# Kernel optimization log

Measured on AMD Instinct MI355X. Metric: run time of the kernel, lower is better.

Reference implementation:

```python
import jax, jax.numpy as jnp
import numpy as np

N = 50000      # nodes
E = 800000     # edges (before self-loops)
IN = 128
HID = 128
OUT = 64
L = 8          # num_layers
ALPHA = 0.1
THETA = 0.5
BN_EPS = 1e-5


def setup_inputs() -> dict:
    key = jax.random.key(0)
    ks = jax.random.split(key, 8)
    x = jax.random.normal(ks[0], (N, IN), dtype=jnp.float32)
    edge_index = jax.random.randint(ks[1], (2, E), 0, N, dtype=jnp.int32)
    # nn.Linear default init: U(-1/sqrt(fan_in), 1/sqrt(fan_in))
    s0 = 1.0 / np.sqrt(IN)
    lin0_w = jax.random.uniform(ks[2], (HID, IN), jnp.float32, -s0, s0)
    lin0_b = jax.random.uniform(ks[3], (HID,), jnp.float32, -s0, s0)
    s1 = 1.0 / np.sqrt(HID)
    lin1_w = jax.random.uniform(ks[4], (OUT, HID), jnp.float32, -s1, s1)
    lin1_b = jax.random.uniform(ks[5], (OUT,), jnp.float32, -s1, s1)
    # GCN2Conv weight1: glorot, shape [HID, HID], applied as h @ W
    g = np.sqrt(6.0 / (HID + HID))
    conv_w = jax.random.uniform(ks[6], (L, HID, HID), jnp.float32, -g, g)
    bn_gamma = jnp.ones((L, HID), jnp.float32)
    bn_beta = jnp.zeros((L, HID), jnp.float32)
    return {"x": x, "edge_index": edge_index, "lin0_w": lin0_w, "lin0_b": lin0_b,
            "lin1_w": lin1_w, "lin1_b": lin1_b, "conv_w": conv_w,
            "bn_gamma": bn_gamma, "bn_beta": bn_beta}


def _gcn_norm(edge_index):
    """PyG gcn_norm with add_self_loops=True, improved=False."""
    loops = jnp.arange(N, dtype=edge_index.dtype)
    src = jnp.concatenate([edge_index[0], loops])
    dst = jnp.concatenate([edge_index[1], loops])
    w = jnp.ones(src.shape[0], jnp.float32)
    deg = jax.ops.segment_sum(w, dst, num_segments=N)
    dinv = jnp.where(deg > 0, jax.lax.rsqrt(jnp.maximum(deg, 1e-12)), 0.0)
    norm = dinv[src] * w * dinv[dst]
    return src, dst, norm


def reference(x, edge_index, lin0_w, lin0_b, lin1_w, lin1_b, conv_w, bn_gamma, bn_beta):
    src, dst, norm = _gcn_norm(edge_index)
    # input projection (dropout is identity in eval/reference mode)
    h = jax.nn.relu(x @ lin0_w.T + lin0_b)
    h0 = h
    for i in range(L):
        # sparse adjacency propagation: out[dst] += norm * h[src]
        agg = jax.ops.segment_sum(norm[:, None] * h[src], dst, num_segments=N)
        # GCN2Conv with shared weights, normalize=False
        z = (1.0 - ALPHA) * agg + ALPHA * h0
        beta = float(np.log(THETA / (i + 1) + 1.0))
        z = (1.0 - beta) * z + beta * (z @ conv_w[i])
        # BatchNorm1d over nodes (batch statistics, biased variance)
        mean = z.mean(axis=0)
        var = z.var(axis=0)
        z = (z - mean) * jax.lax.rsqrt(var + BN_EPS) * bn_gamma[i] + bn_beta[i]
        h = jax.nn.relu(z)
    return h @ lin1_w.T + lin1_b
```

## Files before the change

kernel.cpp:

```cpp
#include <hip/hip_runtime.h>
#include <hip/hip_bf16.h>
#include <math.h>

#define N_NODES 50000
#define N_EDGES 800000
#define NLAYERS 8
#define ALPHA_C 0.1f
#define BN_EPS  1e-5f

typedef unsigned short u16;
typedef __attribute__((ext_vector_type(8))) short short8;
typedef __attribute__((ext_vector_type(4))) float f32x4;

static __device__ __forceinline__ u16 f2bf(float f) {
    unsigned u = __float_as_uint(f);
    unsigned r = (u + 0x7fffu + ((u >> 16) & 1u)) >> 16;
    return (u16)r;
}
static __device__ __forceinline__ float bf2f(u16 b) {
    return __uint_as_float((unsigned)b << 16);
}

__global__ __launch_bounds__(256) void k_init(int* cnt, int* fill, float* stats) {
    int i = blockIdx.x * 256 + threadIdx.x;
    if (i < N_NODES) { cnt[i] = 0; fill[i] = 0; }
    if (i < NLAYERS * 256) stats[i] = 0.0f;
}

__global__ __launch_bounds__(256) void k_count(const int* __restrict__ dst, int* cnt) {
    int e = blockIdx.x * 256 + threadIdx.x;
    if (e < N_EDGES) atomicAdd(&cnt[dst[e]], 1);
}

__global__ __launch_bounds__(256) void k_dinv(const int* __restrict__ cnt, float* __restrict__ dinv) {
    int i = blockIdx.x * 256 + threadIdx.x;
    if (i < N_NODES) dinv[i] = rsqrtf((float)(cnt[i] + 1));
}

__global__ __launch_bounds__(1024) void k_scan_local(const int* __restrict__ cnt,
                                                     int* __restrict__ rowptr, int* __restrict__ bsum) {
    __shared__ int tmp[1024];
    int t = threadIdx.x;
    int i = blockIdx.x * 1024 + t;
    int v = (i < N_NODES) ? cnt[i] : 0;
    tmp[t] = v;
    __syncthreads();
    for (int off = 1; off < 1024; off <<= 1) {
        int y = (t >= off) ? tmp[t - off] : 0;
        __syncthreads();
        tmp[t] += y;
        __syncthreads();
    }
    if (i < N_NODES) rowptr[i] = tmp[t] - v;
    if (t == 1023) bsum[blockIdx.x] = tmp[t];
}

__global__ void k_scan_top(int* bsum) {
    __shared__ int tmp[64];
    int t = threadIdx.x;
    int v = (t < 49) ? bsum[t] : 0;
    tmp[t] = v;
    __syncthreads();
    for (int off = 1; off < 64; off <<= 1) {
        int y = (t >= off) ? tmp[t - off] : 0;
        __syncthreads();
        tmp[t] += y;
        __syncthreads();
    }
    if (t < 49) bsum[t] = tmp[t] - v;
}

__global__ __launch_bounds__(256) void k_scan_add(int* __restrict__ rowptr, const int* __restrict__ bsum) {
    int i = blockIdx.x * 256 + threadIdx.x;
    if (i < N_NODES) rowptr[i] += bsum[i >> 10];
    if (i == 0) rowptr[N_NODES] = N_EDGES;
}

__global__ __launch_bounds__(256) void k_scatter(const int* __restrict__ src, const int* __restrict__ dst,
                                                 const int* __restrict__ rowptr, int* fill,
                                                 u16* __restrict__ ssrc) {
    int e = blockIdx.x * 256 + threadIdx.x;
    if (e < N_EDGES) {
        int d = dst[e];
        int pos = rowptr[d] + atomicAdd(&fill[d], 1);
        ssrc[pos] = (u16)src[e];
    }
}

__global__ __launch_bounds__(256) void k_convw(const float* __restrict__ conv_w,
                                               const float* __restrict__ lin0_w,
                                               const float* __restrict__ lin1_w,
                                               u16* __restrict__ wtb) {
    int t = blockIdx.x * 256 + threadIdx.x;
    if (t < 131072) {
        int j = (t >> 7) & 127, k = t & 127;
        int i = t >> 14;
        float v = conv_w[(i << 14) + (k << 7) + j];
        wtb[(t & ~127) | (k ^ ((j & 7) << 3))] = f2bf(v);
    } else if (t < 131072 + 16384) {
        int u = t - 131072;
        int j = u >> 7, k = u & 127;
        wtb[131072 + ((u & ~127) | (k ^ ((j & 7) << 3)))] = f2bf(lin0_w[u]);
    } else if (t < 131072 + 16384 + 8192) {
        int u = t - 147456;
        int j = u >> 7, k = u & 127;
        wtb[147456 + ((u & ~127) | (k ^ ((j & 7) << 3)))] = f2bf(lin1_w[u]);
    }
}

__global__ __launch_bounds__(256) void k_convx(const float* __restrict__ x, u16* __restrict__ xb) {
    size_t i = ((size_t)blockIdx.x * 256 + threadIdx.x) * 4;
    int row = (int)(i >> 7), j = (int)(i & 127);
    float4 v = *(const float4*)(x + i);
    uint2 o;
    o.x = (unsigned)f2bf(v.x) | ((unsigned)f2bf(v.y) << 16);
    o.y = (unsigned)f2bf(v.z) | ((unsigned)f2bf(v.w) << 16);
    *(uint2*)(xb + ((size_t)(j >> 4) * N_NODES + row) * 16 + (j & 15)) = o;
}

template<int NT, int MODE>
__global__ __launch_bounds__(256) void k_gemm_mfma(const u16* __restrict__ A,
                                                   const u16* __restrict__ Wg,
                                                   const float* __restrict__ bias,
                                                   float* __restrict__ Zf,
                                                   u16* __restrict__ h0b,
                                                   u16* __restrict__ hbp,
                                                   float* __restrict__ outF,
                                                   float* __restrict__ stats,
                                                   const float* __restrict__ dinv,
                                                   float beta_c, int M) {
    __shared__ u16 Ws[NT * 16 * 128];
    __shared__ float sstat[256];
    int tid = threadIdx.x;

    {
        const float4* srcv = (const float4*)Wg;
        float4* dstv = (float4*)Ws;
#pragma unroll
        for (int i = 0; i < NT; ++i) dstv[tid + i * 256] = srcv[tid + i * 256];
    }
    if (MODE == 1) sstat[tid] = 0.f;

    int wave = tid >> 6, lane = tid & 63;
    int r0 = blockIdx.x * 64 + wave * 16;
    int kg = lane >> 4;
    int cl = lane & 15;

    int arow = r0 + cl;
    int acl = arow < M ? arow : M - 1;
    short8 afrag[4];
#pragma unroll
    for (int kk = 0; kk < 4; ++kk) {
        int s = kk * 2 + (kg >> 1);
        afrag[kk] = *(const short8*)(A + ((size_t)s * N_NODES + acl) * 16 + (kg & 1) * 8);
    }

    __syncthreads();

    f32x4 acc[NT];
#pragma unroll
    for (int nt = 0; nt < NT; ++nt) {
        acc[nt] = (f32x4){0.f, 0.f, 0.f, 0.f};
        int j = nt * 16 + cl;
        const u16* wrow = Ws + j * 128;
        int sw = (j & 7) << 3;
#pragma unroll
        for (int kk = 0; kk < 4; ++kk) {
            short8 b = *(const short8*)(wrow + ((kk * 32 + kg * 8) ^ sw));
            acc[nt] = __builtin_amdgcn_mfma_f32_16x16x32_bf16(afrag[kk], b, acc[nt], 0, 0, 0);
        }
    }

    int rbase = r0 + kg * 4;
    float dvr[4];
    if (MODE != 1) {
#pragma unroll
        for (int reg = 0; reg < 4; ++reg) {
            int row = rbase + reg;
            dvr[reg] = (row < M) ? dinv[row] : 1.f;
        }
    }

#pragma unroll
    for (int nt = 0; nt < NT; ++nt) {
        int j = nt * 16 + cl;
        float s = 0.f, ss = 0.f;
#pragma unroll
        for (int reg = 0; reg < 4; ++reg) {
            int row = rbase + reg;
            if (row >= M) continue;
            float v = acc[nt][reg];
            size_t idx = ((size_t)nt * N_NODES + row) * 16 + cl;
            if (MODE == 0) {
                v = fmaxf(v + bias[j], 0.f);
                h0b[idx] = f2bf(v);
                hbp[idx] = f2bf(v * dvr[reg]);
            } else if (MODE == 1) {
                float zin = bf2f(A[idx]);
                v = (1.0f - beta_c) * zin + beta_c * v;
                Zf[idx] = v;
                s += v;
                ss = fmaf(v, v, ss);
            } else {
                outF[(size_t)row * (NT * 16) + j] = v / dvr[reg] + bias[j];
            }
        }
        if (MODE == 1) {
            s  += __shfl_xor(s, 16);  s  += __shfl_xor(s, 32);
            ss += __shfl_xor(ss, 16); ss += __shfl_xor(ss, 32);
            if (kg == 0) {
                atomicAdd(&sstat[j], s);
                atomicAdd(&sstat[128 + j], ss);
            }
        }
    }
    if (MODE == 1) {
        __syncthreads();
        atomicAdd(&stats[tid], sstat[tid]);
    }
}

__global__ __launch_bounds__(256) void k_aggregate(const u16* __restrict__ hbp, const u16* __restrict__ h0b,
                                                   const int* __restrict__ rowptr, const u16* __restrict__ ssrc,
                                                   const float* __restrict__ dinv,
                                                   u16* __restrict__ Zb) {
    int slice = blockIdx.x & 7;
    int wave = threadIdx.x >> 6, lane = threadIdx.x & 63;
    int rg = lane >> 3, lg = lane & 7;
    int v = (blockIdx.x >> 3) * 32 + wave * 8 + rg;
    if (v >= N_NODES) return;
    const u16* hs = hbp + (size_t)slice * (N_NODES * 16);
    int beg = rowptr[v], end = rowptr[v + 1];

    float ax, ay;
    {
        unsigned u = *(const unsigned*)(hs + (size_t)v * 16 + lg * 2);
        ax = __uint_as_float(u << 16);
        ay = __uint_as_float(u & 0xffff0000u);
    }
    int p = beg;
    for (; p + 4 <= end; p += 4) {
        int s0 = ssrc[p], s1 = ssrc[p + 1], s2 = ssrc[p + 2], s3 = ssrc[p + 3];
        unsigned u0 = *(const unsigned*)(hs + (size_t)s0 * 16 + lg * 2);
        unsigned u1 = *(const unsigned*)(hs + (size_t)s1 * 16 + lg * 2);
        unsigned u2 = *(const unsigned*)(hs + (size_t)s2 * 16 + lg * 2);
        unsigned u3 = *(const unsigned*)(hs + (size_t)s3 * 16 + lg * 2);
        ax += __uint_as_float(u0 << 16); ay += __uint_as_float(u0 & 0xffff0000u);
        ax += __uint_as_float(u1 << 16); ay += __uint_as_float(u1 & 0xffff0000u);
        ax += __uint_as_float(u2 << 16); ay += __uint_as_float(u2 & 0xffff0000u);
        ax += __uint_as_float(u3 << 16); ay += __uint_as_float(u3 & 0xffff0000u);
    }
    for (; p < end; ++p) {
        int s = ssrc[p];
        unsigned u = *(const unsigned*)(hs + (size_t)s * 16 + lg * 2);
        ax += __uint_as_float(u << 16); ay += __uint_as_float(u & 0xffff0000u);
    }

    float dv = dinv[v];
    unsigned uh = *(const unsigned*)(h0b + ((size_t)slice * N_NODES + v) * 16 + lg * 2);
    float zx = (1.0f - ALPHA_C) * dv * ax + ALPHA_C * __uint_as_float(uh << 16);
    float zy = (1.0f - ALPHA_C) * dv * ay + ALPHA_C * __uint_as_float(uh & 0xffff0000u);
    *(unsigned*)(Zb + ((size_t)slice * N_NODES + v) * 16 + lg * 2) =
        (unsigned)f2bf(zx) | ((unsigned)f2bf(zy) << 16);
}

__global__ __launch_bounds__(256) void k_bn_relu(const float* __restrict__ Zf, const float* __restrict__ stats,
                                                 const float* __restrict__ gamma, const float* __restrict__ betap,
                                                 const float* __restrict__ dinv, u16* __restrict__ hbp) {
    __shared__ float ssc[128], ssh[128];
    int t = threadIdx.x;
    if (t < 128) {
        float mean = stats[t] * (1.0f / N_NODES);
        float var = stats[128 + t] * (1.0f / N_NODES) - mean * mean;
        float istd = rsqrtf(var + BN_EPS);
        float sc = gamma[t] * istd;
        ssc[t] = sc;
        ssh[t] = betap[t] - mean * sc;
    }
    __syncthreads();
    int e4 = blockIdx.x * 256 + t;
    if (e4 >= N_NODES * 32) return;
    int slice = e4 / (N_NODES * 4);
    int rem = e4 - slice * (N_NODES * 4);
    int row = rem >> 2;
    int j0 = slice * 16 + (rem & 3) * 4;
    float dv = dinv[row];
    float4 z = *(const float4*)(Zf + (size_t)e4 * 4);
    float r0 = fmaxf(fmaf(z.x, ssc[j0 + 0], ssh[j0 + 0]), 0.f) * dv;
    float r1 = fmaxf(fmaf(z.y, ssc[j0 + 1], ssh[j0 + 1]), 0.f) * dv;
    float r2 = fmaxf(fmaf(z.z, ssc[j0 + 2], ssh[j0 + 2]), 0.f) * dv;
    float r3 = fmaxf(fmaf(z.w, ssc[j0 + 3], ssh[j0 + 3]), 0.f) * dv;
    uint2 o;
    o.x = (unsigned)f2bf(r0) | ((unsigned)f2bf(r1) << 16);
    o.y = (unsigned)f2bf(r2) | ((unsigned)f2bf(r3) << 16);
    *(uint2*)(hbp + (size_t)e4 * 4) = o;
}


extern "C" void kernel_launch(void* const* d_in, const int* in_sizes, int n_in,
                              void* d_out, int out_size, void* d_ws, size_t ws_size,
                              hipStream_t stream) {
    const float* x      = (const float*)d_in[0];
    const int*   ei     = (const int*)d_in[1];
    const float* lin0_w = (const float*)d_in[2];
    const float* lin0_b = (const float*)d_in[3];
    const float* lin1_w = (const float*)d_in[4];
    const float* lin1_b = (const float*)d_in[5];
    const float* conv_w = (const float*)d_in[6];
    const float* bn_g   = (const float*)d_in[7];
    const float* bn_b   = (const float*)d_in[8];
    const int* e_src = ei;
    const int* e_dst = ei + N_EDGES;

    char* p = (char*)d_ws;
    auto alloc = [&](size_t bytes) -> void* {
        void* r = (void*)p;
        p += (bytes + 255) & ~(size_t)255;
        return r;
    };
    int*   cnt    = (int*)alloc((size_t)N_NODES * 4);
    int*   rowptr = (int*)alloc((size_t)(N_NODES + 1) * 4);
    int*   fill   = (int*)alloc((size_t)N_NODES * 4);
    float* dinv   = (float*)alloc((size_t)N_NODES * 4);
    u16*   ssrc   = (u16*)alloc((size_t)N_EDGES * 2);
    int*   bsum   = (int*)alloc(64 * 4);
    u16*   h0b    = (u16*)alloc((size_t)N_NODES * 128 * 2);
    float* Zf     = (float*)alloc((size_t)N_NODES * 128 * 4);
    u16*   Zb     = (u16*)alloc((size_t)N_NODES * 128 * 2);
    u16*   hbp    = (u16*)alloc((size_t)N_NODES * 128 * 2);
    u16*   wtb    = (u16*)alloc((size_t)(131072 + 16384 + 8192) * 2);
    float* stats  = (float*)alloc((size_t)NLAYERS * 256 * 4);

    const int nblk = (N_NODES + 255) / 256;
    const int eblk = (N_EDGES + 255) / 256;
    const int gblk = (N_NODES + 63) / 64;
    const int vblk = N_NODES * 128 / 4 / 256;
    const int ablk = ((N_NODES + 31) / 32) * 8;
    const int bnblk = (N_NODES * 32 + 255) / 256;

    k_init<<<nblk, 256, 0, stream>>>(cnt, fill, stats);
    k_count<<<eblk, 256, 0, stream>>>(e_dst, cnt);
    k_dinv<<<nblk, 256, 0, stream>>>(cnt, dinv);
    k_scan_local<<<49, 1024, 0, stream>>>(cnt, rowptr, bsum);
    k_scan_top<<<1, 64, 0, stream>>>(bsum);
    k_scan_add<<<196, 256, 0, stream>>>(rowptr, bsum);
    k_scatter<<<eblk, 256, 0, stream>>>(e_src, e_dst, rowptr, fill, ssrc);
    k_convw<<<(131072 + 16384 + 8192 + 255) / 256, 256, 0, stream>>>(conv_w, lin0_w, lin1_w, wtb);
    k_convx<<<vblk, 256, 0, stream>>>(x, Zb);

    k_gemm_mfma<8, 0><<<gblk, 256, 0, stream>>>(Zb, wtb + 131072, lin0_b, nullptr, h0b, hbp, nullptr, nullptr, dinv, 0.f, N_NODES);

    for (int i = 0; i < NLAYERS; ++i) {
        k_aggregate<<<ablk, 256, 0, stream>>>(hbp, h0b, rowptr, ssrc, dinv, Zb);
        float beta = (float)log(0.5 / (double)(i + 1) + 1.0);
        k_gemm_mfma<8, 1><<<gblk, 256, 0, stream>>>(Zb, wtb + (size_t)i * 16384, nullptr, Zf, nullptr, nullptr, nullptr, stats + (size_t)i * 256, nullptr, beta, N_NODES);
        k_bn_relu<<<bnblk, 256, 0, stream>>>(Zf, stats + (size_t)i * 256, bn_g + i * 128, bn_b + i * 128, dinv, hbp);
    }

    k_gemm_mfma<4, 2><<<gblk, 256, 0, stream>>>(hbp, wtb + 147456, lin1_b, nullptr, nullptr, nullptr, (float*)d_out, nullptr, dinv, 0.f, N_NODES);
}
```

Baseline: 870.7 us.

## Sort nodes by degree and widen per-lane aggregation loads to 16 bytes

Adds a degree-binning counting sort that builds a node permutation, so the lanes of a wave aggregate nodes with similar in-degree and less time is lost to divergence. The aggregation kernel now gives each node two lanes that each load 16 bytes (8 bf16 features) instead of eight lanes loading 4 bytes, which cuts the number of gather instructions and index loads per edge. The cost is three extra setup kernels, a perm indirection per node, fewer lanes per gather (less memory-level parallelism per node), and scattered output writes.

```diff
diff --git a/kernel.cpp b/kernel.cpp
--- a/kernel.cpp
+++ b/kernel.cpp
@@ -20,11 +20,14 @@
 static __device__ __forceinline__ float bf2f(u16 b) {
     return __uint_as_float((unsigned)b << 16);
 }
-
-__global__ __launch_bounds__(256) void k_init(int* cnt, int* fill, float* stats) {
+static __device__ __forceinline__ float blo(unsigned w) { return __uint_as_float(w << 16); }
+static __device__ __forceinline__ float bhi(unsigned w) { return __uint_as_float(w & 0xffff0000u); }
+
+__global__ __launch_bounds__(256) void k_init(int* cnt, int* fill, float* stats, int* bins, int* binfill) {
     int i = blockIdx.x * 256 + threadIdx.x;
     if (i < N_NODES) { cnt[i] = 0; fill[i] = 0; }
     if (i < NLAYERS * 256) stats[i] = 0.0f;
+    if (i < 64) { bins[i] = 0; binfill[i] = 0; }
 }
 
 __global__ __launch_bounds__(256) void k_count(const int* __restrict__ dst, int* cnt) {
@@ -35,6 +38,41 @@
 __global__ __launch_bounds__(256) void k_dinv(const int* __restrict__ cnt, float* __restrict__ dinv) {
     int i = blockIdx.x * 256 + threadIdx.x;
     if (i < N_NODES) dinv[i] = rsqrtf((float)(cnt[i] + 1));
+}
+
+__global__ __launch_bounds__(256) void k_bin(const int* __restrict__ cnt, int* bins) {
+    __shared__ int h[64];
+    if (threadIdx.x < 64) h[threadIdx.x] = 0;
+    __syncthreads();
+    int i = blockIdx.x * 256 + threadIdx.x;
+    if (i < N_NODES) atomicAdd(&h[min(cnt[i], 63)], 1);
+    __syncthreads();
+    if (threadIdx.x < 64 && h[threadIdx.x]) atomicAdd(&bins[threadIdx.x], h[threadIdx.x]);
+}
+
+__global__ void k_binscan(int* bins) {
+    __shared__ int tmp[64];
+    int t = threadIdx.x;
+    int v = bins[t];
+    tmp[t] = v;
+    __syncthreads();
+    for (int off = 1; off < 64; off <<= 1) {
+        int y = (t >= off) ? tmp[t - off] : 0;
+        __syncthreads();
+        tmp[t] += y;
+        __syncthreads();
+    }
+    bins[t] = tmp[t] - v;
+}
+
+__global__ __launch_bounds__(256) void k_perm(const int* __restrict__ cnt, const int* __restrict__ binoff,
+                                              int* binfill, int* __restrict__ perm) {
+    int i = blockIdx.x * 256 + threadIdx.x;
+    if (i < N_NODES) {
+        int b = min(cnt[i], 63);
+        int pos = binoff[b] + atomicAdd(&binfill[b], 1);
+        perm[pos] = i;
+    }
 }
 
 __global__ __launch_bounds__(1024) void k_scan_local(const int* __restrict__ cnt,
@@ -222,46 +260,63 @@
 
 __global__ __launch_bounds__(256) void k_aggregate(const u16* __restrict__ hbp, const u16* __restrict__ h0b,
                                                    const int* __restrict__ rowptr, const u16* __restrict__ ssrc,
-                                                   const float* __restrict__ dinv,
+                                                   const float* __restrict__ dinv, const int* __restrict__ perm,
                                                    u16* __restrict__ Zb) {
     int slice = blockIdx.x & 7;
     int wave = threadIdx.x >> 6, lane = threadIdx.x & 63;
-    int rg = lane >> 3, lg = lane & 7;
-    int v = (blockIdx.x >> 3) * 32 + wave * 8 + rg;
-    if (v >= N_NODES) return;
-    const u16* hs = hbp + (size_t)slice * (N_NODES * 16);
+    int rg = lane >> 1, hf = lane & 1;
+    int idx = (blockIdx.x >> 3) * 128 + wave * 32 + rg;
+    if (idx >= N_NODES) return;
+    int v = perm[idx];
+    const u16* hs = hbp + (size_t)slice * ((size_t)N_NODES * 16);
     int beg = rowptr[v], end = rowptr[v + 1];
 
-    float ax, ay;
+    float a0, a1, a2, a3, a4, a5, a6, a7;
     {
-        unsigned u = *(const unsigned*)(hs + (size_t)v * 16 + lg * 2);
-        ax = __uint_as_float(u << 16);
-        ay = __uint_as_float(u & 0xffff0000u);
+        uint4 u = *(const uint4*)(hs + (size_t)v * 16 + hf * 8);
+        a0 = blo(u.x); a1 = bhi(u.x); a2 = blo(u.y); a3 = bhi(u.y);
+        a4 = blo(u.z); a5 = bhi(u.z); a6 = blo(u.w); a7 = bhi(u.w);
     }
     int p = beg;
     for (; p + 4 <= end; p += 4) {
         int s0 = ssrc[p], s1 = ssrc[p + 1], s2 = ssrc[p + 2], s3 = ssrc[p + 3];
-        unsigned u0 = *(const unsigned*)(hs + (size_t)s0 * 16 + lg * 2);
-        unsigned u1 = *(const unsigned*)(hs + (size_t)s1 * 16 + lg * 2);
-        unsigned u2 = *(const unsigned*)(hs + (size_t)s2 * 16 + lg * 2);
-        unsigned u3 = *(const unsigned*)(hs + (size_t)s3 * 16 + lg * 2);
-        ax += __uint_as_float(u0 << 16); ay += __uint_as_float(u0 & 0xffff0000u);
-        ax += __uint_as_float(u1 << 16); ay += __uint_as_float(u1 & 0xffff0000u);
-        ax += __uint_as_float(u2 << 16); ay += __uint_as_float(u2 & 0xffff0000u);
-        ax += __uint_as_float(u3 << 16); ay += __uint_as_float(u3 & 0xffff0000u);
+        uint4 u0 = *(const uint4*)(hs + (size_t)s0 * 16 + hf * 8);
+        uint4 u1 = *(const uint4*)(hs + (size_t)s1 * 16 + hf * 8);
+        uint4 u2 = *(const uint4*)(hs + (size_t)s2 * 16 + hf * 8);
+        uint4 u3 = *(const uint4*)(hs + (size_t)s3 * 16 + hf * 8);
+        a0 += blo(u0.x); a1 += bhi(u0.x); a2 += blo(u0.y); a3 += bhi(u0.y);
+        a4 += blo(u0.z); a5 += bhi(u0.z); a6 += blo(u0.w); a7 += bhi(u0.w);
+        a0 += blo(u1.x); a1 += bhi(u1.x); a2 += blo(u1.y); a3 += bhi(u1.y);
+        a4 += blo(u1.z); a5 += bhi(u1.z); a6 += blo(u1.w); a7 += bhi(u1.w);
+        a0 += blo(u2.x); a1 += bhi(u2.x); a2 += blo(u2.y); a3 += bhi(u2.y);
+        a4 += blo(u2.z); a5 += bhi(u2.z); a6 += blo(u2.w); a7 += bhi(u2.w);
+        a0 += blo(u3.x); a1 += bhi(u3.x); a2 += blo(u3.y); a3 += bhi(u3.y);
+        a4 += blo(u3.z); a5 += bhi(u3.z); a6 += blo(u3.w); a7 += bhi(u3.w);
     }
     for (; p < end; ++p) {
         int s = ssrc[p];
-        unsigned u = *(const unsigned*)(hs + (size_t)s * 16 + lg * 2);
-        ax += __uint_as_float(u << 16); ay += __uint_as_float(u & 0xffff0000u);
-    }
-
-    float dv = dinv[v];
-    unsigned uh = *(const unsigned*)(h0b + ((size_t)slice * N_NODES + v) * 16 + lg * 2);
-    float zx = (1.0f - ALPHA_C) * dv * ax + ALPHA_C * __uint_as_float(uh << 16);
-    float zy = (1.0f - ALPHA_C) * dv * ay + ALPHA_C * __uint_as_float(uh & 0xffff0000u);
-    *(unsigned*)(Zb + ((size_t)slice * N_NODES + v) * 16 + lg * 2) =
-        (unsigned)f2bf(zx) | ((unsigned)f2bf(zy) << 16);
+        uint4 u = *(const uint4*)(hs + (size_t)s * 16 + hf * 8);
+        a0 += blo(u.x); a1 += bhi(u.x); a2 += blo(u.y); a3 += bhi(u.y);
+        a4 += blo(u.z); a5 += bhi(u.z); a6 += blo(u.w); a7 += bhi(u.w);
+    }
+
+    float dv = dinv[v] * (1.0f - ALPHA_C);
+    size_t oidx = ((size_t)slice * N_NODES + v) * 16 + hf * 8;
+    uint4 uh = *(const uint4*)(h0b + oidx);
+    float z0 = dv * a0 + ALPHA_C * blo(uh.x);
+    float z1 = dv * a1 + ALPHA_C * bhi(uh.x);
+    float z2 = dv * a2 + ALPHA_C * blo(uh.y);
+    float z3 = dv * a3 + ALPHA_C * bhi(uh.y);
+    float z4 = dv * a4 + ALPHA_C * blo(uh.z);
+    float z5 = dv * a5 + ALPHA_C * bhi(uh.z);
+    float z6 = dv * a6 + ALPHA_C * blo(uh.w);
+    float z7 = dv * a7 + ALPHA_C * bhi(uh.w);
+    uint4 o;
+    o.x = (unsigned)f2bf(z0) | ((unsigned)f2bf(z1) << 16);
+    o.y = (unsigned)f2bf(z2) | ((unsigned)f2bf(z3) << 16);
+    o.z = (unsigned)f2bf(z4) | ((unsigned)f2bf(z5) << 16);
+    o.w = (unsigned)f2bf(z6) | ((unsigned)f2bf(z7) << 16);
+    *(uint4*)(Zb + oidx) = o;
 }
 
 __global__ __launch_bounds__(256) void k_bn_relu(const float* __restrict__ Zf, const float* __restrict__ stats,
@@ -324,6 +379,9 @@
     float* dinv   = (float*)alloc((size_t)N_NODES * 4);
     u16*   ssrc   = (u16*)alloc((size_t)N_EDGES * 2);
     int*   bsum   = (int*)alloc(64 * 4);
+    int*   bins   = (int*)alloc(64 * 4);
+    int*   binfill= (int*)alloc(64 * 4);
+    int*   perm   = (int*)alloc((size_t)N_NODES * 4);
     u16*   h0b    = (u16*)alloc((size_t)N_NODES * 128 * 2);
     float* Zf     = (float*)alloc((size_t)N_NODES * 128 * 4);
     u16*   Zb     = (u16*)alloc((size_t)N_NODES * 128 * 2);
@@ -335,12 +393,15 @@
     const int eblk = (N_EDGES + 255) / 256;
     const int gblk = (N_NODES + 63) / 64;
     const int vblk = N_NODES * 128 / 4 / 256;
-    const int ablk = ((N_NODES + 31) / 32) * 8;
+    const int ablk = ((N_NODES + 127) / 128) * 8;
     const int bnblk = (N_NODES * 32 + 255) / 256;
 
-    k_init<<<nblk, 256, 0, stream>>>(cnt, fill, stats);
+    k_init<<<nblk, 256, 0, stream>>>(cnt, fill, stats, bins, binfill);
     k_count<<<eblk, 256, 0, stream>>>(e_dst, cnt);
     k_dinv<<<nblk, 256, 0, stream>>>(cnt, dinv);
+    k_bin<<<nblk, 256, 0, stream>>>(cnt, bins);
+    k_binscan<<<1, 64, 0, stream>>>(bins);
+    k_perm<<<nblk, 256, 0, stream>>>(cnt, bins, binfill, perm);
     k_scan_local<<<49, 1024, 0, stream>>>(cnt, rowptr, bsum);
     k_scan_top<<<1, 64, 0, stream>>>(bsum);
     k_scan_add<<<196, 256, 0, stream>>>(rowptr, bsum);
@@ -351,7 +412,7 @@
     k_gemm_mfma<8, 0><<<gblk, 256, 0, stream>>>(Zb, wtb + 131072, lin0_b, nullptr, h0b, hbp, nullptr, nullptr, dinv, 0.f, N_NODES);
 
     for (int i = 0; i < NLAYERS; ++i) {
-        k_aggregate<<<ablk, 256, 0, stream>>>(hbp, h0b, rowptr, ssrc, dinv, Zb);
+        k_aggregate<<<ablk, 256, 0, stream>>>(hbp, h0b, rowptr, ssrc, dinv, perm, Zb);
         float beta = (float)log(0.5 / (double)(i + 1) + 1.0);
         k_gemm_mfma<8, 1><<<gblk, 256, 0, stream>>>(Zb, wtb + (size_t)i * 16384, nullptr, Zf, nullptr, nullptr, nullptr, stats + (size_t)i * 256, nullptr, beta, N_NODES);
         k_bn_relu<<<bnblk, 256, 0, stream>>>(Zf, stats + (size_t)i * 256, bn_g + i * 128, bn_b + i * 128, dinv, hbp);
```

Result: slower. 1.089 ms (+25.1%).
